# Kernel optimization log

Hardware: AMD Instinct MI355X
Metric: run time of the kernel (lower is better)

The kernel has to match this reference:

```python
import jax, jax.numpy as jnp
import numpy as np

N = 100000
E = 1000000
F = 64
H = 64
G = 64  # number of graphs
EPS = 1e-5


def setup_inputs() -> dict:
    key = jax.random.key(0)
    ks = jax.random.split(key, 12)
    x = jax.random.normal(ks[0], (N, F), dtype=jnp.float32)
    edge_index = jax.random.randint(ks[1], (2, E), 0, N, dtype=jnp.int32)
    batch = jnp.sort(jax.random.randint(ks[2], (N,), 0, G, dtype=jnp.int32))
    s1 = 1.0 / np.sqrt(F)
    s2 = 1.0 / np.sqrt(H)
    inp = {
        "x": x,
        "edge_index": edge_index,
        "batch": batch,
        # GCNConv layers (weight [out,in] like torch Linear, bias [out])
        "W1": jax.random.uniform(ks[3], (H, F), jnp.float32, -s1, s1),
        "b1": jnp.zeros((H,), jnp.float32),
        "W2": jax.random.uniform(ks[4], (H, H), jnp.float32, -s2, s2),
        "b2": jnp.zeros((H,), jnp.float32),
        # BatchNorm (eval mode: running stats)
        "bn1_g": jnp.ones((H,), jnp.float32),
        "bn1_b": jnp.zeros((H,), jnp.float32),
        "bn1_m": jax.random.normal(ks[5], (H,), jnp.float32) * 0.1,
        "bn1_v": jax.random.uniform(ks[6], (H,), jnp.float32, 0.5, 1.5),
        "bn2_g": jnp.ones((H,), jnp.float32),
        "bn2_b": jnp.zeros((H,), jnp.float32),
        "bn2_m": jax.random.normal(ks[7], (H,), jnp.float32) * 0.1,
        "bn2_v": jax.random.uniform(ks[8], (H,), jnp.float32, 0.5, 1.5),
        # MLP head
        "lin1_W": jax.random.uniform(ks[9], (H // 2, H), jnp.float32, -s2, s2),
        "lin1_b": jnp.zeros((H // 2,), jnp.float32),
        "lin2_W": jax.random.uniform(ks[10], (1, H // 2), jnp.float32, -1.0 / np.sqrt(H // 2), 1.0 / np.sqrt(H // 2)),
        "lin2_b": jnp.zeros((1,), jnp.float32),
    }
    return inp


def _gcn_norm(edge_index):
    # PyG GCNConv default: add self-loops, symmetric normalization
    loop = jnp.arange(N, dtype=edge_index.dtype)
    row = jnp.concatenate([edge_index[0], loop])  # source
    col = jnp.concatenate([edge_index[1], loop])  # target
    deg = jax.ops.segment_sum(jnp.ones_like(col, jnp.float32), col, num_segments=N)
    dinv = jnp.where(deg > 0, jax.lax.rsqrt(deg), 0.0)
    norm = dinv[row] * dinv[col]  # [E+N]
    return row, col, norm


def _gcn_conv(x, W, b, row, col, norm):
    h = x @ W.T                       # [N, H] transform first (cheap)
    msg = h[row] * norm[:, None]      # [E+N, H] gather + scale
    out = jax.ops.segment_sum(msg, col, num_segments=N)  # scatter-add
    return out + b


def _bn_eval(x, g, b, m, v):
    return (x - m) * (g * jax.lax.rsqrt(v + EPS)) + b


def reference(x, edge_index, batch, W1, b1, W2, b2,
              bn1_g, bn1_b, bn1_m, bn1_v, bn2_g, bn2_b, bn2_m, bn2_v,
              lin1_W, lin1_b, lin2_W, lin2_b):
    row, col, norm = _gcn_norm(edge_index)
    # layer 1: conv -> BN -> relu (dropout inactive in eval)
    h = _gcn_conv(x, W1, b1, row, col, norm)
    h = jax.nn.relu(_bn_eval(h, bn1_g, bn1_b, bn1_m, bn1_v))
    # layer 2
    h = _gcn_conv(h, W2, b2, row, col, norm)
    h = jax.nn.relu(_bn_eval(h, bn2_g, bn2_b, bn2_m, bn2_v))
    # global mean pool over graphs
    sums = jax.ops.segment_sum(h, batch, num_segments=G)          # [G, H]
    cnt = jax.ops.segment_sum(jnp.ones((N,), h.dtype), batch, num_segments=G)
    pooled = sums / jnp.maximum(cnt, 1.0)[:, None]
    # MLP head
    z = jax.nn.relu(pooled @ lin1_W.T + lin1_b)
    return z @ lin2_W.T + lin2_b  # [G, 1]
```

## Files before the change

kernel.cpp:

```cpp
#include <hip/hip_runtime.h>
#include <math.h>

#define EPS_BN 1e-5f
#define CAP 48
#define BINSHIFT 9
#define EDGESHIFT 12
#define NBUCK_MAX 199

__device__ __forceinline__ float4 pull_fixed_d(const float4* __restrict__ h4, const float* __restrict__ dinv,
                                               const int* __restrict__ icnt, const int* __restrict__ csr,
                                               int i, int q) {
    int deg = icnt[i];
    float di = dinv[i];
    float4 acc = h4[i * 16 + q];
    float dd = di * di;
    acc.x *= dd; acc.y *= dd; acc.z *= dd; acc.w *= dd;
    int degc = min(deg, CAP);
    int base = i * CAP;
    int kend = base + ((degc + 3) & ~3);
    if (base < kend) {
        int4 rr = *(const int4*)(csr + base);
        for (int k = base; k < kend; k += 4) {
            int4 cur = rr;
            if (k + 4 < kend) rr = *(const int4*)(csr + k + 4);
            float w0 = dinv[cur.x] * di;
            float w1 = dinv[cur.y] * di;
            float w2 = dinv[cur.z] * di;
            float w3 = dinv[cur.w] * di;
            float4 v0 = h4[cur.x * 16 + q];
            float4 v1 = h4[cur.y * 16 + q];
            float4 v2 = h4[cur.z * 16 + q];
            float4 v3 = h4[cur.w * 16 + q];
            acc.x += v0.x * w0 + v1.x * w1 + v2.x * w2 + v3.x * w3;
            acc.y += v0.y * w0 + v1.y * w1 + v2.y * w2 + v3.y * w3;
            acc.z += v0.z * w0 + v1.z * w1 + v2.z * w2 + v3.z * w3;
            acc.w += v0.w * w0 + v1.w * w1 + v2.w * w2 + v3.w * w3;
        }
    }
    return acc;
}

__device__ __forceinline__ float4 pull_plain_d(const float4* __restrict__ h4, const int* __restrict__ icnt,
                                               const float* __restrict__ dinv,
                                               const int* __restrict__ csr, int i, int q) {
    int deg = icnt[i];
    float4 acc = h4[i * 16 + q];
    int degc = min(deg, CAP);
    int base = i * CAP;
    int kend = base + ((degc + 3) & ~3);
    if (base < kend) {
        int4 rr = *(const int4*)(csr + base);
        for (int k = base; k < kend; k += 4) {
            int4 cur = rr;
            if (k + 4 < kend) rr = *(const int4*)(csr + k + 4);
            float4 v0 = h4[cur.x * 16 + q];
            float4 v1 = h4[cur.y * 16 + q];
            float4 v2 = h4[cur.z * 16 + q];
            float4 v3 = h4[cur.w * 16 + q];
            acc.x += v0.x + v1.x + v2.x + v3.x;
            acc.y += v0.y + v1.y + v2.y + v3.y;
            acc.z += v0.z + v1.z + v2.z + v3.z;
            acc.w += v0.w + v1.w + v2.w + v3.w;
        }
    }
    float di = dinv[i];
    acc.x *= di; acc.y *= di; acc.z *= di; acc.w *= di;
    return acc;
}

__global__ __launch_bounds__(256) void k_binit(int nblka,
    const int* __restrict__ row, const int* __restrict__ col, int e, int nbuck,
    int2* __restrict__ regions, int* __restrict__ offs, int n,
    int* icnt, float* dinv, float* gsum, float* gcnt, float* rowA, float* rowB,
    const float* b1, const float* g1, const float* bb1, const float* m1, const float* v1,
    const float* b2, const float* g2, const float* bb2, const float* m2, const float* v2,
    float* sc1, float* sh1, float* sc2, float* sh2) {
    __shared__ __align__(16) char smem[34816];
    int t = threadIdx.x;
    if ((int)blockIdx.x < nblka) {
        int2* so = (int2*)smem;
        int* soff = (int*)(smem + 32768);
        int* sfill = soff + 256;
        int blk = blockIdx.x;
        int base = blk << EDGESHIFT;
        int nE = min(1 << EDGESHIFT, e - base);

        int r4[16], c4[16];
        int j0 = t * 16;
        int m = nE - j0; m = m < 0 ? 0 : (m > 16 ? 16 : m);
        if (m == 16) {
#pragma unroll
            for (int cc = 0; cc < 4; ++cc) {
                int4 a = *(const int4*)(row + base + j0 + 4 * cc);
                int4 b = *(const int4*)(col + base + j0 + 4 * cc);
                r4[4 * cc] = a.x; r4[4 * cc + 1] = a.y; r4[4 * cc + 2] = a.z; r4[4 * cc + 3] = a.w;
                c4[4 * cc] = b.x; c4[4 * cc + 1] = b.y; c4[4 * cc + 2] = b.z; c4[4 * cc + 3] = b.w;
            }
        } else {
            for (int j = 0; j < m; ++j) { r4[j] = row[base + j0 + j]; c4[j] = col[base + j0 + j]; }
        }
        if (t < nbuck) { soff[t] = 0; sfill[t] = 0; }
        __syncthreads();
        for (int j = 0; j < m; ++j) atomicAdd(&soff[c4[j] >> BINSHIFT], 1);
        __syncthreads();
        for (int d = 1; d < nbuck; d <<= 1) {
            int add = 0;
            if (t < nbuck && t >= d) add = soff[t - d];
            __syncthreads();
            if (t < nbuck) soff[t] += add;
            __syncthreads();
        }
        for (int j = 0; j < m; ++j) {
            int bk = c4[j] >> BINSHIFT;
            int pos = (bk ? soff[bk - 1] : 0) + atomicAdd(&sfill[bk], 1);
            so[pos] = make_int2(r4[j], c4[j]);
        }
        __syncthreads();
        int4* gdst = (int4*)(regions + ((size_t)blk << EDGESHIFT));
        const int4* lsrc = (const int4*)so;
#pragma unroll
        for (int k = 0; k < 8; ++k) gdst[t + 256 * k] = lsrc[t + 256 * k];
        if (t <= nbuck) offs[blk * 200 + t] = (t == 0) ? 0 : soff[t - 1];
    } else {
        int gtid = (blockIdx.x - nblka) * 256 + t;
        if (gtid < 4096) gsum[gtid] = 0.0f;
        if (gtid < 64) { gcnt[gtid] = 0.0f; rowA[gtid] = 0.0f; rowB[gtid] = 0.0f; }
        if (gtid >= 64 && gtid < 68) icnt[n + gtid - 64] = 0;
        if (gtid >= 68 && gtid < 72) dinv[n + gtid - 68] = 1.0f;
        if (gtid >= 128 && gtid < 192) {
            int tt = gtid - 128;
            float s1 = g1[tt] / sqrtf(v1[tt] + EPS_BN);
            sc1[tt] = s1;
            sh1[tt] = (b1[tt] - m1[tt]) * s1 + bb1[tt];
            float s2 = g2[tt] / sqrtf(v2[tt] + EPS_BN);
            sc2[tt] = s2;
            sh2[tt] = (b2[tt] - m2[tt]) * s2 + bb2[tt];
        }
    }
}

__global__ __launch_bounds__(256) void k_gemm1build(int nbuild,
    const float* __restrict__ in, const float* __restrict__ W, float* __restrict__ out, int n,
    const int2* __restrict__ regions, const int* __restrict__ offs, int nba,
    int* __restrict__ icnt, float* __restrict__ dinv, int* __restrict__ csr) {
    __shared__ __align__(16) char smem[50176];
    int t = threadIdx.x;
    if ((int)blockIdx.x < nbuild) {
        int* lcsr = (int*)smem;
        int* lcnt = (int*)(smem + 256 * CAP * 4);
        int blk = blockIdx.x;
        int b = blk >> 1, s = blk & 1;
        int node0 = (b << BINSHIFT) + s * 256;
        if (node0 >= n) return;
        for (int idx = t; idx < 256 * CAP; idx += 256) lcsr[idx] = n;
        lcnt[t] = 0;
        __syncthreads();
        for (int r = t; r < nba; r += 256) {
            int o0 = offs[r * 200 + b];
            int o1 = offs[r * 200 + b + 1];
            const int2* reg = regions + ((size_t)r << EDGESHIFT);
            if (o0 < o1) {
                int2 eg = reg[o0];
                for (int k = o0; k < o1; ++k) {
                    int2 cur = eg;
                    if (k + 1 < o1) eg = reg[k + 1];
                    unsigned c = (unsigned)(cur.y - node0);
                    if (c < 256u) {
                        int u = atomicAdd(&lcnt[c], 1);
                        if (u < CAP) lcsr[c * CAP + u] = cur.x;
                    }
                }
            }
        }
        __syncthreads();
        int nv = min(256, n - node0);
        for (int idx = t; idx < nv * CAP; idx += 256) csr[(size_t)node0 * CAP + idx] = lcsr[idx];
        if (t < nv) {
            int d = lcnt[t];
            icnt[node0 + t] = d;
            dinv[node0 + t] = rsqrtf((float)(d + 1));
        }
    } else {
        float4* sx = (float4*)smem;
        float4* Wl = (float4*)(smem + 32768);
        const float4* W4 = (const float4*)W;
        for (int i = t; i < 1024; i += 256) Wl[i] = W4[i];
        int tile = blockIdx.x - nbuild;
        int rbase = tile * 128;
        const float4* in4 = (const float4*)in;
#pragma unroll
        for (int k = 0; k < 8; ++k) {
            int idx = t + k * 256;
            int r = idx >> 4, c = idx & 15;
            int gr = rbase + r;
            float4 v = (gr < n) ? in4[gr * 16 + c] : float4{0.f, 0.f, 0.f, 0.f};
            sx[(r << 4) | (c ^ ((r >> 1) & 15))] = v;
        }
        __syncthreads();
        int hg = t >> 6;
        int h0 = hg * 16;
        int ng = t & 63;
        int n0 = rbase + 2 * ng;
        int sw = ng & 15;
        float acc[2][16];
#pragma unroll
        for (int j = 0; j < 2; ++j)
#pragma unroll
            for (int k = 0; k < 16; ++k) acc[j][k] = 0.0f;
        for (int f4 = 0; f4 < 16; ++f4) {
            float4 xv[2];
#pragma unroll
            for (int j = 0; j < 2; ++j) xv[j] = sx[((2 * ng + j) << 4) | (f4 ^ sw)];
#pragma unroll
            for (int hh = 0; hh < 16; ++hh) {
                float4 w = Wl[(h0 + hh) * 16 + f4];
#pragma unroll
                for (int j = 0; j < 2; ++j) {
                    acc[j][hh] += xv[j].x * w.x;
                    acc[j][hh] += xv[j].y * w.y;
                    acc[j][hh] += xv[j].z * w.z;
                    acc[j][hh] += xv[j].w * w.w;
                }
            }
        }
        float4* out4 = (float4*)out;
#pragma unroll
        for (int j = 0; j < 2; ++j) {
            if (n0 + j >= n) continue;
#pragma unroll
            for (int q = 0; q < 4; ++q) {
                float4 o = {acc[j][4 * q], acc[j][4 * q + 1], acc[j][4 * q + 2], acc[j][4 * q + 3]};
                out4[(n0 + j) * 16 + (h0 >> 2) + q] = o;
            }
        }
    }
}

__global__ __launch_bounds__(256) void k_applygemm2(
    const float* __restrict__ h, const int* __restrict__ icnt, const float* __restrict__ dinv,
    const int* __restrict__ csr, const float* __restrict__ W,
    const float* __restrict__ scale, const float* __restrict__ shift,
    float* __restrict__ out, int n) {
    __shared__ __align__(16) char smem[33280];
    float4* sx = (float4*)smem;
    float4* Wl = (float4*)(smem + 16384);
    float4* scl = (float4*)(smem + 32768);
    float4* shl = scl + 16;
    int t = threadIdx.x;
    const float4* W4 = (const float4*)W;
    for (int i = t; i < 1024; i += 256) Wl[i] = W4[i];
    if (t < 16) {
        scl[t] = ((const float4*)scale)[t];
        shl[t] = ((const float4*)shift)[t];
    }
    int rbase = blockIdx.x * 64;
    for (int k = 0; k < 4; ++k) {
        int idx = t + k * 256;
        int r = idx >> 4, q = idx & 15;
        int i = rbase + r;
        float4 acc = {0.f, 0.f, 0.f, 0.f};
        if (i < n) acc = pull_fixed_d((const float4*)h, dinv, icnt, csr, i, q);
        sx[(r << 4) | (q ^ ((r >> 1) & 15))] = acc;
    }
    __syncthreads();
    int hg = t >> 6;
    int h0 = hg * 16;
    int ng = t & 63;
    int n0 = rbase + ng;
    int sw = (ng >> 1) & 15;
    float acc[16];
#pragma unroll
    for (int k = 0; k < 16; ++k) acc[k] = 0.0f;
    for (int f4 = 0; f4 < 16; ++f4) {
        float4 sc = scl[f4], sh = shl[f4];
        float4 v = sx[(ng << 4) | (f4 ^ sw)];
        v.x = fmaxf(v.x * sc.x + sh.x, 0.0f);
        v.y = fmaxf(v.y * sc.y + sh.y, 0.0f);
        v.z = fmaxf(v.z * sc.z + sh.z, 0.0f);
        v.w = fmaxf(v.w * sc.w + sh.w, 0.0f);
#pragma unroll
        for (int hh = 0; hh < 16; ++hh) {
            float4 w = Wl[(h0 + hh) * 16 + f4];
            acc[hh] += v.x * w.x;
            acc[hh] += v.y * w.y;
            acc[hh] += v.z * w.z;
            acc[hh] += v.w * w.w;
        }
    }
    if (n0 < n) {
        float di = dinv[n0];
        float4* out4 = (float4*)out;
#pragma unroll
        for (int q = 0; q < 4; ++q) {
            float4 o = {acc[4 * q] * di, acc[4 * q + 1] * di,
                        acc[4 * q + 2] * di, acc[4 * q + 3] * di};
            out4[n0 * 16 + (h0 >> 2) + q] = o;
        }
    }
}

__global__ __launch_bounds__(256) void k_applypool_f(
    const float* __restrict__ h, const int* __restrict__ icnt, const float* __restrict__ dinv,
    const int* __restrict__ csr, const int* __restrict__ batch,
    const float* __restrict__ sc, const float* __restrict__ sh,
    float* gsum, float* gcnt, int n) {
    __shared__ float spart[64 * 64];
    __shared__ float scnt[64];
    int node0 = blockIdx.x * 128;
    int last = min(node0 + 127, n - 1);
    int g0 = batch[node0];
    int rc = batch[last] - g0 + 1;
    for (int idx = threadIdx.x; idx < rc * 64; idx += 256) spart[idx] = 0.0f;
    if (threadIdx.x < rc) scnt[threadIdx.x] = 0.0f;
    __syncthreads();
    int q = threadIdx.x & 15;
    float4 s4 = ((const float4*)sc)[q];
    float4 b4 = ((const float4*)sh)[q];
    for (int it = 0; it < 8; ++it) {
        int i = node0 + it * 16 + (threadIdx.x >> 4);
        if (i < n) {
            float4 acc = pull_plain_d((const float4*)h, icnt, dinv, csr, i, q);
            acc.x = fmaxf(acc.x * s4.x + b4.x, 0.0f);
            acc.y = fmaxf(acc.y * s4.y + b4.y, 0.0f);
            acc.z = fmaxf(acc.z * s4.z + b4.z, 0.0f);
            acc.w = fmaxf(acc.w * s4.w + b4.w, 0.0f);
            int gl = batch[i] - g0;
            float* pp = &spart[gl * 64 + q * 4];
            atomicAdd(pp + 0, acc.x);
            atomicAdd(pp + 1, acc.y);
            atomicAdd(pp + 2, acc.z);
            atomicAdd(pp + 3, acc.w);
            if (q == 0) atomicAdd(&scnt[gl], 1.0f);
        }
    }
    __syncthreads();
    for (int idx = threadIdx.x; idx < rc * 64; idx += 256) {
        int gl = idx >> 6, f = idx & 63;
        atomicAdd(&gsum[(g0 + gl) * 64 + f], spart[idx]);
    }
    if (threadIdx.x < rc) atomicAdd(&gcnt[g0 + threadIdx.x], scnt[threadIdx.x]);
}

__global__ void k_mlp(const float* __restrict__ gsum, const float* __restrict__ gcnt,
                      const float* __restrict__ l1W, const float* __restrict__ l1b,
                      const float* __restrict__ l2W, const float* __restrict__ l2b,
                      float* __restrict__ outp) {
    int g = threadIdx.x;
    if (g >= 64) return;
    float inv = 1.0f / fmaxf(gcnt[g], 1.0f);
    float p[64];
#pragma unroll
    for (int hh = 0; hh < 64; ++hh) p[hh] = gsum[g * 64 + hh] * inv;
    float o = l2b[0];
    for (int j = 0; j < 32; ++j) {
        float a = l1b[j];
#pragma unroll
        for (int hh = 0; hh < 64; ++hh) a += p[hh] * l1W[j * 64 + hh];
        o += fmaxf(a, 0.0f) * l2W[j];
    }
    outp[g] = o;
}

extern "C" void kernel_launch(void* const* d_in, const int* in_sizes, int n_in,
                              void* d_out, int out_size, void* d_ws, size_t ws_size,
                              hipStream_t stream) {
    const int N = in_sizes[0] / 64;
    const int E = in_sizes[1] / 2;

    const float* x    = (const float*)d_in[0];
    const int*  row   = (const int*)d_in[1];
    const int*  colp  = ((const int*)d_in[1]) + E;
    const int*  batch = (const int*)d_in[2];
    const float* W1   = (const float*)d_in[3];
    const float* b1   = (const float*)d_in[4];
    const float* W2   = (const float*)d_in[5];
    const float* b2   = (const float*)d_in[6];
    const float* bn1g = (const float*)d_in[7];
    const float* bn1b = (const float*)d_in[8];
    const float* bn1m = (const float*)d_in[9];
    const float* bn1v = (const float*)d_in[10];
    const float* bn2g = (const float*)d_in[11];
    const float* bn2b = (const float*)d_in[12];
    const float* bn2m = (const float*)d_in[13];
    const float* bn2v = (const float*)d_in[14];
    const float* l1W  = (const float*)d_in[15];
    const float* l1b  = (const float*)d_in[16];
    const float* l2W  = (const float*)d_in[17];
    const float* l2b  = (const float*)d_in[18];
    float* out = (float*)d_out;

    int* icnt = (int*)d_ws;
    float* dinv = (float*)(icnt + N + 4);
    float* sc1 = dinv + N + 4;
    float* sh1 = sc1 + 64;
    float* sc2 = sh1 + 64;
    float* sh2 = sc2 + 64;
    float* gsum = sh2 + 64;
    float* gcnt = gsum + 4096;
    int* csr = (int*)(gcnt + 64);
    float* bufA = (float*)(csr + (size_t)N * CAP);
    float* bufB = bufA + (size_t)(N + 1) * 64;

    const int NBLKA = (E + (1 << EDGESHIFT) - 1) >> EDGESHIFT;
    const int NBUCK = (N + 511) >> BINSHIFT;
    int2* regions = (int2*)bufB;
    int* offs = (int*)(regions + ((size_t)NBLKA << EDGESHIFT));

    int nbg     = (N + 127) / 128;
    int nb_ag2  = (N + 63) / 64;
    int nb_apl  = (N + 127) / 128;
    int nbuild  = NBUCK * 2;

    k_binit<<<NBLKA + 16, 256, 0, stream>>>(NBLKA, row, colp, E, NBUCK, regions, offs, N,
                                            icnt, dinv, gsum, gcnt,
                                            bufA + (size_t)N * 64, bufB + (size_t)N * 64,
                                            b1, bn1g, bn1b, bn1m, bn1v,
                                            b2, bn2g, bn2b, bn2m, bn2v,
                                            sc1, sh1, sc2, sh2);
    k_gemm1build<<<nbuild + nbg, 256, 0, stream>>>(nbuild, x, W1, bufA, N,
                                                   regions, offs, NBLKA, icnt, dinv, csr);
    k_applygemm2<<<nb_ag2, 256, 0, stream>>>(bufA, icnt, dinv, csr, W2, sc1, sh1, bufB, N);
    k_applypool_f<<<nb_apl, 256, 0, stream>>>(bufB, icnt, dinv, csr, batch, sc2, sh2, gsum, gcnt, N);
    k_mlp<<<1, 64, 0, stream>>>(gsum, gcnt, l1W, l1b, l2W, l2b, out);
}
```

Before: 291.5 us.

## Interleave CSR build and GEMM blocks; use nontemporal loads for edge streams

Switches CSR index and edge-region loads to nontemporal loads so streamed index data is less likely to evict the reused feature rows from cache. It also interleaves the build blocks and GEMM tiles by block id, so the memory-latency-bound build work and the compute-bound GEMM work are co-scheduled across CUs rather than run as two separate phases. The block mapping assumes the GEMM tile count is at least nbuild; if it is not, some block ids map to tiles past the end of the input.

```diff
diff --git a/kernel.cpp b/kernel.cpp
--- a/kernel.cpp
+++ b/kernel.cpp
@@ -6,6 +6,17 @@
 #define BINSHIFT 9
 #define EDGESHIFT 12
 #define NBUCK_MAX 199
+
+__device__ __forceinline__ int4 ntload_i4(const int* p) {
+    typedef int iv4 __attribute__((ext_vector_type(4)));
+    iv4 v = __builtin_nontemporal_load((const iv4*)p);
+    return int4{v.x, v.y, v.z, v.w};
+}
+__device__ __forceinline__ int2 ntload_i2(const int2* p) {
+    typedef int iv2 __attribute__((ext_vector_type(2)));
+    iv2 v = __builtin_nontemporal_load((const iv2*)p);
+    return make_int2(v.x, v.y);
+}
 
 __device__ __forceinline__ float4 pull_fixed_d(const float4* __restrict__ h4, const float* __restrict__ dinv,
                                                const int* __restrict__ icnt, const int* __restrict__ csr,
@@ -19,10 +30,10 @@
     int base = i * CAP;
     int kend = base + ((degc + 3) & ~3);
     if (base < kend) {
-        int4 rr = *(const int4*)(csr + base);
+        int4 rr = ntload_i4(csr + base);
         for (int k = base; k < kend; k += 4) {
             int4 cur = rr;
-            if (k + 4 < kend) rr = *(const int4*)(csr + k + 4);
+            if (k + 4 < kend) rr = ntload_i4(csr + k + 4);
             float w0 = dinv[cur.x] * di;
             float w1 = dinv[cur.y] * di;
             float w2 = dinv[cur.z] * di;
@@ -49,10 +60,10 @@
     int base = i * CAP;
     int kend = base + ((degc + 3) & ~3);
     if (base < kend) {
-        int4 rr = *(const int4*)(csr + base);
+        int4 rr = ntload_i4(csr + base);
         for (int k = base; k < kend; k += 4) {
             int4 cur = rr;
-            if (k + 4 < kend) rr = *(const int4*)(csr + k + 4);
+            if (k + 4 < kend) rr = ntload_i4(csr + k + 4);
             float4 v0 = h4[cur.x * 16 + q];
             float4 v1 = h4[cur.y * 16 + q];
             float4 v2 = h4[cur.z * 16 + q];
@@ -145,10 +156,12 @@
     int* __restrict__ icnt, float* __restrict__ dinv, int* __restrict__ csr) {
     __shared__ __align__(16) char smem[50176];
     int t = threadIdx.x;
-    if ((int)blockIdx.x < nbuild) {
+    int bid = blockIdx.x;
+    bool isbuild = (bid < 2 * nbuild) && (bid & 1);
+    if (isbuild) {
         int* lcsr = (int*)smem;
         int* lcnt = (int*)(smem + 256 * CAP * 4);
-        int blk = blockIdx.x;
+        int blk = bid >> 1;
         int b = blk >> 1, s = blk & 1;
         int node0 = (b << BINSHIFT) + s * 256;
         if (node0 >= n) return;
@@ -160,10 +173,10 @@
             int o1 = offs[r * 200 + b + 1];
             const int2* reg = regions + ((size_t)r << EDGESHIFT);
             if (o0 < o1) {
-                int2 eg = reg[o0];
+                int2 eg = ntload_i2(reg + o0);
                 for (int k = o0; k < o1; ++k) {
                     int2 cur = eg;
-                    if (k + 1 < o1) eg = reg[k + 1];
+                    if (k + 1 < o1) eg = ntload_i2(reg + k + 1);
                     unsigned c = (unsigned)(cur.y - node0);
                     if (c < 256u) {
                         int u = atomicAdd(&lcnt[c], 1);
@@ -185,7 +198,7 @@
         float4* Wl = (float4*)(smem + 32768);
         const float4* W4 = (const float4*)W;
         for (int i = t; i < 1024; i += 256) Wl[i] = W4[i];
-        int tile = blockIdx.x - nbuild;
+        int tile = (bid < 2 * nbuild) ? (bid >> 1) : (bid - nbuild);
         int rbase = tile * 128;
         const float4* in4 = (const float4*)in;
 #pragma unroll
```

Measured after the change: 334.8 us. 1.15x slower.
